# Optimization experiments

Measured on AMD Instinct MI355X. Metric: run time of the kernel, lower is better.

## Reference

```python
import jax, jax.numpy as jnp
import numpy as np

B, S, D = 4, 2048, 1024  # batch, seq_len, input_dim == output_dim (dk)


def setup_inputs() -> dict:
    key = jax.random.key(0)
    kx, kq, kk, kv = jax.random.split(key, 4)
    # xavier_uniform bound for square [D, D] matrices
    bound = float(np.sqrt(6.0 / (D + D)))
    return {
        "x": jax.random.normal(kx, (B, S, D), dtype=jnp.float32),
        "WQ": jax.random.uniform(kq, (D, D), jnp.float32, -bound, bound),
        "WK": jax.random.uniform(kk, (D, D), jnp.float32, -bound, bound),
        "WV": jax.random.uniform(kv, (D, D), jnp.float32, -bound, bound),
    }


def reference(x, WQ, WK, WV):
    dk = WQ.shape[1]
    q = x @ WQ  # [B, S, dk]
    k = x @ WK
    v = x @ WV
    scores = jnp.einsum("bsd,btd->bst", q, k) / jnp.sqrt(jnp.asarray(dk, x.dtype))
    # causal mask: tril ones -> positions where mask==0 set to -inf
    s = x.shape[1]
    causal = jnp.tril(jnp.ones((s, s), dtype=bool))
    scores = jnp.where(causal[None, :, :], scores, jnp.asarray(-jnp.inf, x.dtype))
    attention = jax.nn.softmax(scores, axis=-1)
    # NOTE: original applies attention_dropout to `scores` post-softmax and
    # discards the result -> dead op; eval-mode output is attention @ v.
    return jnp.einsum("bst,btd->bsd", attention, v)
```

## Files before the change

kernel.cpp:

```cpp
#include <hip/hip_runtime.h>
#include <stdint.h>


typedef unsigned short u16;
typedef __attribute__((ext_vector_type(8))) short shortx8;
typedef __attribute__((ext_vector_type(4))) float floatx4;

static constexpr int BB = 4;
static constexpr int SS = 2048;
static constexpr int DD = 1024;

__device__ __forceinline__ u16 f2bf(float f) {
  union { float f; uint32_t u; } c; c.f = f;
  uint32_t u = c.u;
  return (u16)((u + 0x7fffu + ((u >> 16) & 1u)) >> 16);
}

__device__ __forceinline__ float bfhi2f(uint32_t u) {
  union { uint32_t u; float f; } c; c.u = u & 0xffff0000u; return c.f;
}
__device__ __forceinline__ float bflo2f(uint32_t u) {
  union { uint32_t u; float f; } c; c.u = u << 16; return c.f;
}

#define GLOAD_LDS16(g, l)                                                              \
  __builtin_amdgcn_global_load_lds((const __attribute__((address_space(1))) void*)(g), \
                                   (__attribute__((address_space(3))) void*)(l), 16, 0, 0)

__device__ __forceinline__ void gemm_core_128(
    const u16* __restrict__ A, const u16* __restrict__ Bt,
    int lda, int ldb, int m0, int n0, int kend, floatx4 acc[4][4])
{
  __shared__ u16 lA[128 * 64];
  __shared__ u16 lB[128 * 64];
  const int t = threadIdx.x;
  const int w = t >> 6, l = t & 63;
  const int wm = w >> 1, wn = w & 1;
  const int sr = l >> 3;
  const int scq = ((l & 7) ^ (l >> 3)) * 8;

#pragma unroll
  for (int i = 0; i < 4; ++i)
#pragma unroll
    for (int j = 0; j < 4; ++j)
      acc[i][j] = (floatx4){0.f, 0.f, 0.f, 0.f};

  const u16* Ab = A + (size_t)m0 * lda;
  const u16* Bb = Bt + (size_t)n0 * ldb;

  for (int k0 = 0; k0 < kend; k0 += 64) {
#pragma unroll
    for (int i = 0; i < 4; ++i) {
      const int row = w * 32 + i * 8;
      GLOAD_LDS16(Ab + (size_t)(row + sr) * lda + k0 + scq, &lA[row * 64]);
      GLOAD_LDS16(Bb + (size_t)(row + sr) * ldb + k0 + scq, &lB[row * 64]);
    }
    __syncthreads();

#pragma unroll
    for (int ks = 0; ks < 2; ++ks) {
      const int ca = ((ks * 4 + (l >> 4)) ^ (l & 7)) * 8;
      shortx8 af[4], bf[4];
#pragma unroll
      for (int i = 0; i < 4; ++i)
        af[i] = *(const shortx8*)&lA[(wm * 64 + i * 16 + (l & 15)) * 64 + ca];
#pragma unroll
      for (int i = 0; i < 4; ++i)
        bf[i] = *(const shortx8*)&lB[(wn * 64 + i * 16 + (l & 15)) * 64 + ca];
#pragma unroll
      for (int i = 0; i < 4; ++i)
#pragma unroll
        for (int j = 0; j < 4; ++j)
          acc[i][j] = __builtin_amdgcn_mfma_f32_16x16x32_bf16(af[i], bf[j], acc[i][j], 0, 0, 0);
    }
    __syncthreads();
  }
}

__global__ __launch_bounds__(256) void prep(const float* __restrict__ x,
                                            const float* __restrict__ WQ,
                                            const float* __restrict__ WK,
                                            const float* __restrict__ WV,
                                            u16* __restrict__ xb,
                                            u16* __restrict__ Wt) {
  __shared__ float tile[64][65];
  const int bid = blockIdx.x;
  const int t = threadIdx.x;
  if (bid < 8192) {
    const size_t i = (size_t)bid * 256 + t;
    float4 v = ((const float4*)x)[i];
    ushort4 o;
    o.x = f2bf(v.x); o.y = f2bf(v.y); o.z = f2bf(v.z); o.w = f2bf(v.w);
    ((ushort4*)xb)[i] = o;
    return;
  }
  const int r = bid - 8192;
  const int wsel = r >> 8;
  const int rr = r & 255;
  const int k0 = (rr >> 4) * 64, n0 = (rr & 15) * 64;
  const float* W = wsel == 0 ? WQ : (wsel == 1 ? WK : WV);
  const int tx = t & 63, ty = t >> 6;
#pragma unroll
  for (int i = 0; i < 16; ++i)
    tile[ty + i * 4][tx] = W[(size_t)(k0 + ty + i * 4) * DD + n0 + tx];
  __syncthreads();
  u16* dst = Wt + (size_t)wsel * DD * DD;
#pragma unroll
  for (int i = 0; i < 16; ++i)
    dst[(size_t)(n0 + ty + i * 4) * DD + k0 + tx] = f2bf(tile[tx][ty + i * 4]);
}

__global__ __launch_bounds__(256, 2) void qkv_gemm(const u16* __restrict__ x,
                                                   const u16* __restrict__ Wt,
                                                   u16* __restrict__ Q,
                                                   u16* __restrict__ K,
                                                   u16* __restrict__ Vt) {
  const int m0 = blockIdx.x * 128;
  const int n0t = blockIdx.y * 128;
  floatx4 acc[4][4];
  gemm_core_128(x, Wt, DD, DD, m0, n0t, DD, acc);

  const int t = threadIdx.x, w = t >> 6, l = t & 63;
  const int wm = w >> 1, wn = w & 1;

  if (n0t >= 2048) {
    const int bb = m0 >> 11;
    const int s0 = (m0 & 2047) + wm * 64 + (l >> 4) * 4;
    u16* vt = Vt + (size_t)bb * DD * SS;
#pragma unroll
    for (int i = 0; i < 4; ++i)
#pragma unroll
      for (int j = 0; j < 4; ++j) {
        const int n = (n0t - 2048) + wn * 64 + j * 16 + (l & 15);
        const int s = s0 + i * 16;
        ushort4 o4;
        o4.x = f2bf(acc[i][j][0]);
        o4.y = f2bf(acc[i][j][1]);
        o4.z = f2bf(acc[i][j][2]);
        o4.w = f2bf(acc[i][j][3]);
        *(ushort4*)(vt + (size_t)n * SS + s) = o4;
      }
    return;
  }

  u16* out = (n0t < 1024) ? Q : K;
  const int n0 = n0t & 1023;
#pragma unroll
  for (int i = 0; i < 4; ++i)
#pragma unroll
    for (int j = 0; j < 4; ++j)
#pragma unroll
      for (int r = 0; r < 4; ++r) {
        const int m = m0 + wm * 64 + i * 16 + (l >> 4) * 4 + r;
        const int n = n0 + wn * 64 + j * 16 + (l & 15);
        out[(size_t)m * DD + n] = f2bf(acc[i][j][r]);
      }
}

__global__ __launch_bounds__(256, 2) void scores_gemm(const u16* __restrict__ Q,
                                                      const u16* __restrict__ Kt,
                                                      u16* __restrict__ Scb) {
  const int b = blockIdx.z;
  const int tcode = blockIdx.x;
  int mb = (int)((sqrtf(8.0f * (float)tcode + 1.0f) - 1.0f) * 0.5f);
  while ((mb + 1) * (mb + 2) / 2 <= tcode) ++mb;
  while (mb * (mb + 1) / 2 > tcode) --mb;
  const int nb = tcode - mb * (mb + 1) / 2;
  const int m0 = mb * 128, n0 = nb * 128;

  floatx4 acc[4][4];
  gemm_core_128(Q + (size_t)b * SS * DD, Kt + (size_t)b * SS * DD, DD, DD, m0, n0, DD, acc);

  u16* out = Scb + (size_t)b * SS * SS;
  const int t = threadIdx.x, w = t >> 6, l = t & 63;
  const int wm = w >> 1, wn = w & 1;
#pragma unroll
  for (int i = 0; i < 4; ++i)
#pragma unroll
    for (int j = 0; j < 4; ++j)
#pragma unroll
      for (int r = 0; r < 4; ++r) {
        const int m = m0 + wm * 64 + i * 16 + (l >> 4) * 4 + r;
        const int n = n0 + wn * 64 + j * 16 + (l & 15);
        out[(size_t)m * SS + n] = f2bf(acc[i][j][r] * 0.03125f);
      }
}

__global__ __launch_bounds__(256) void softmax_causal(const u16* __restrict__ Scb,
                                                      u16* __restrict__ P) {
  const int row = blockIdx.x * 4 + (threadIdx.x >> 6);
  const int l = threadIdx.x & 63;
  const int b = row >> 11, i = row & 2047;
  const u16* s = Scb + (size_t)b * SS * SS + (size_t)i * SS;
  u16* p = P + (size_t)b * SS * SS + (size_t)i * SS;
  const int n = i + 1;
  const int jend = (i + 128) & ~127;
  const int nc = (jend + 511) >> 9;

  float v[4][8];
  float mx = -INFINITY;
#pragma unroll
  for (int c = 0; c < 4; ++c) {
    if (c < nc) {
      const int col = c * 512 + l * 8;
      uint4 raw = *(const uint4*)(s + col);
      v[c][0] = bflo2f(raw.x); v[c][1] = bfhi2f(raw.x);
      v[c][2] = bflo2f(raw.y); v[c][3] = bfhi2f(raw.y);
      v[c][4] = bflo2f(raw.z); v[c][5] = bfhi2f(raw.z);
      v[c][6] = bflo2f(raw.w); v[c][7] = bfhi2f(raw.w);
#pragma unroll
      for (int e = 0; e < 8; ++e) {
        v[c][e] = (col + e < n) ? v[c][e] : -INFINITY;
        mx = fmaxf(mx, v[c][e]);
      }
    }
  }
#pragma unroll
  for (int o = 32; o > 0; o >>= 1) mx = fmaxf(mx, __shfl_xor(mx, o, 64));

  float sum = 0.f;
#pragma unroll
  for (int c = 0; c < 4; ++c) {
    if (c < nc) {
#pragma unroll
      for (int e = 0; e < 8; ++e) {
        v[c][e] = __expf(v[c][e] - mx);
        sum += v[c][e];
      }
    }
  }
#pragma unroll
  for (int o = 32; o > 0; o >>= 1) sum += __shfl_xor(sum, o, 64);
  const float inv = 1.0f / sum;

#pragma unroll
  for (int c = 0; c < 4; ++c) {
    if (c < nc) {
      const int col = c * 512 + l * 8;
      if (col < jend) {
        uint4 o4;
        o4.x = (uint32_t)f2bf(v[c][0] * inv) | ((uint32_t)f2bf(v[c][1] * inv) << 16);
        o4.y = (uint32_t)f2bf(v[c][2] * inv) | ((uint32_t)f2bf(v[c][3] * inv) << 16);
        o4.z = (uint32_t)f2bf(v[c][4] * inv) | ((uint32_t)f2bf(v[c][5] * inv) << 16);
        o4.w = (uint32_t)f2bf(v[c][6] * inv) | ((uint32_t)f2bf(v[c][7] * inv) << 16);
        *(uint4*)(p + col) = o4;
      }
    }
  }
}

__global__ __launch_bounds__(256, 2) void pv_gemm(const u16* __restrict__ P,
                                                  const u16* __restrict__ Vt,
                                                  float* __restrict__ out) {
  const int b = blockIdx.z;
  const int mb = 15 - blockIdx.y;
  const int m0 = mb * 128, n0 = blockIdx.x * 128;
  floatx4 acc[4][4];
  gemm_core_128(P + (size_t)b * SS * SS, Vt + (size_t)b * DD * SS, SS, SS, m0, n0, m0 + 128, acc);

  float* o = out + (size_t)b * SS * DD;
  const int t = threadIdx.x, w = t >> 6, l = t & 63;
  const int wm = w >> 1, wn = w & 1;
#pragma unroll
  for (int i = 0; i < 4; ++i)
#pragma unroll
    for (int j = 0; j < 4; ++j)
#pragma unroll
      for (int r = 0; r < 4; ++r) {
        const int m = m0 + wm * 64 + i * 16 + (l >> 4) * 4 + r;
        const int n = n0 + wn * 64 + j * 16 + (l & 15);
        o[(size_t)m * DD + n] = acc[i][j][r];
      }
}

extern "C" void kernel_launch(void* const* d_in, const int* in_sizes, int n_in,
                              void* d_out, int out_size, void* d_ws, size_t ws_size,
                              hipStream_t stream) {
  const float* x  = (const float*)d_in[0];
  const float* WQ = (const float*)d_in[1];
  const float* WK = (const float*)d_in[2];
  const float* WV = (const float*)d_in[3];
  float* out = (float*)d_out;

  char* ws = (char*)d_ws;
  const size_t WT_OFF = 0;
  const size_t XB_OFF = WT_OFF + (size_t)3072 * 1024 * 2;
  const size_t Q_OFF  = XB_OFF + (size_t)BB * SS * DD * 2;
  const size_t K_OFF  = Q_OFF + (size_t)BB * SS * DD * 2;
  const size_t VT_OFF = K_OFF + (size_t)BB * SS * DD * 2;
  const size_t P_OFF  = VT_OFF + (size_t)BB * SS * DD * 2;
  const size_t SC_OFF = P_OFF + (size_t)BB * SS * SS * 2;
  u16* Wt  = (u16*)(ws + WT_OFF);
  u16* xb  = (u16*)(ws + XB_OFF);
  u16* Q   = (u16*)(ws + Q_OFF);
  u16* Kb  = (u16*)(ws + K_OFF);
  u16* Vt  = (u16*)(ws + VT_OFF);
  u16* P   = (u16*)(ws + P_OFF);
  u16* Scb = (u16*)(ws + SC_OFF);

  hipLaunchKernelGGL(prep, dim3(8960), dim3(256), 0, stream, x, WQ, WK, WV, xb, Wt);
  hipLaunchKernelGGL(qkv_gemm, dim3(64, 24), dim3(256), 0, stream, xb, Wt, Q, Kb, Vt);
  hipLaunchKernelGGL(scores_gemm, dim3(136, 1, 4), dim3(256), 0, stream, Q, Kb, Scb);
  hipLaunchKernelGGL(softmax_causal, dim3(2048), dim3(256), 0, stream, Scb, P);
  hipLaunchKernelGGL(pv_gemm, dim3(8, 16, 4), dim3(256), 0, stream, P, Vt, out);
}
```

Before: 238.3 us.

## Add 256x256 double-buffered 8-wave GEMM core for QKV and scores kernels

Introduces a 256x256 tile GEMM core with 512 threads, double-buffered LDS staging via global_load_lds, and interleaved quadrant MFMA phases with explicit barriers, waitcnts and setprio. The QKV projection and causal scores kernels switch to it, with grid sizes and the triangular tile indexing adjusted. The goal is more data reuse per tile and overlap of global loads with MFMA work. The cost is 128KB of LDS per block, lower occupancy and coarser causal-tile granularity, which computes more masked work in the scores GEMM.

Result: no change. 239.8 us (+0.6%).

```diff
diff --git a/kernel.cpp b/kernel.cpp
--- a/kernel.cpp
+++ b/kernel.cpp
@@ -23,9 +23,9 @@
   union { uint32_t u; float f; } c; c.u = u << 16; return c.f;
 }
 
-#define GLOAD_LDS16(g, l)                                                              \
-  __builtin_amdgcn_global_load_lds((const __attribute__((address_space(1))) void*)(g), \
-                                   (__attribute__((address_space(3))) void*)(l), 16, 0, 0)
+#define GLOAD_LDS16(g_, l_)                                                             \
+  __builtin_amdgcn_global_load_lds((const __attribute__((address_space(1))) void*)(g_), \
+                                   (__attribute__((address_space(3))) void*)(l_), 16, 0, 0)
 
 __device__ __forceinline__ void gemm_core_128(
     const u16* __restrict__ A, const u16* __restrict__ Bt,
@@ -75,6 +75,132 @@
     }
     __syncthreads();
   }
+}
+
+#define LOAD_AF(mh_)                                                                     \
+  _Pragma("unroll")                                                                      \
+  for (int mi = 0; mi < 4; ++mi)                                                         \
+    _Pragma("unroll")                                                                    \
+    for (int kk = 0; kk < 2; ++kk)                                                       \
+      af[mi][kk] = *(const shortx8*)&As[((mh_) * 128 + wr * 64 + mi * 16 + fr) * 64 +    \
+                                        (((kk * 4 + fq) ^ (l & 7)) * 8)];
+
+#define LOAD_BF(nh_)                                                                     \
+  _Pragma("unroll")                                                                      \
+  for (int ni = 0; ni < 2; ++ni)                                                         \
+    _Pragma("unroll")                                                                    \
+    for (int kk = 0; kk < 2; ++kk)                                                       \
+      bf[ni][kk] = *(const shortx8*)&Bs[((nh_) * 128 + wc * 32 + ni * 16 + fr) * 64 +    \
+                                        (((kk * 4 + fq) ^ (l & 7)) * 8)];
+
+#define MFMA_QUAD(mh_, nh_)                                                              \
+  do {                                                                                   \
+    __builtin_amdgcn_s_setprio(1);                                                       \
+    _Pragma("unroll")                                                                    \
+    for (int mi = 0; mi < 4; ++mi)                                                       \
+      _Pragma("unroll")                                                                  \
+      for (int ni = 0; ni < 2; ++ni)                                                     \
+        _Pragma("unroll")                                                                \
+        for (int kk = 0; kk < 2; ++kk)                                                   \
+          acc[mh_][nh_][mi][ni] = __builtin_amdgcn_mfma_f32_16x16x32_bf16(               \
+              af[mi][kk], bf[ni][kk], acc[mh_][nh_][mi][ni], 0, 0, 0);                   \
+    __builtin_amdgcn_s_setprio(0);                                                       \
+  } while (0)
+
+#define STAGE_A(buf_, half_, k_)                                                         \
+  do {                                                                                   \
+    _Pragma("unroll")                                                                    \
+    for (int j = 0; j < 2; ++j) {                                                        \
+      const int row0 = (half_) * 128 + wv * 16 + j * 8;                                  \
+      GLOAD_LDS16(Ab + (size_t)(row0 + sr) * lda + (k_) + scq, &sm[buf_][0][row0 * 64]); \
+    }                                                                                    \
+  } while (0)
+
+#define STAGE_B(buf_, half_, k_)                                                         \
+  do {                                                                                   \
+    _Pragma("unroll")                                                                    \
+    for (int j = 0; j < 2; ++j) {                                                        \
+      const int row0 = (half_) * 128 + wv * 16 + j * 8;                                  \
+      GLOAD_LDS16(Bb + (size_t)(row0 + sr) * ldb + (k_) + scq, &sm[buf_][1][row0 * 64]); \
+    }                                                                                    \
+  } while (0)
+
+__device__ __forceinline__ void gemm_core_256(
+    const u16* __restrict__ A, const u16* __restrict__ Bt,
+    int lda, int ldb, int m0, int n0, int kend,
+    floatx4 (&acc)[2][2][4][2])
+{
+  __shared__ u16 sm[2][2][256 * 64];
+  const int t = threadIdx.x;
+  const int wv = t >> 6, l = t & 63;
+  const int wr = wv >> 2, wc = wv & 3;
+  const int fr = l & 15, fq = l >> 4;
+  const int sr = l >> 3;
+  const int scq = ((l & 7) ^ sr) * 8;
+
+#pragma unroll
+  for (int a = 0; a < 2; ++a)
+#pragma unroll
+    for (int bq = 0; bq < 2; ++bq)
+#pragma unroll
+      for (int mi = 0; mi < 4; ++mi)
+#pragma unroll
+        for (int ni = 0; ni < 2; ++ni)
+          acc[a][bq][mi][ni] = (floatx4){0.f, 0.f, 0.f, 0.f};
+
+  const u16* Ab = A + (size_t)m0 * lda;
+  const u16* Bb = Bt + (size_t)n0 * ldb;
+  const int T = kend >> 6;
+
+  STAGE_A(0, 0, 0); STAGE_A(0, 1, 0);
+  STAGE_B(0, 0, 0); STAGE_B(0, 1, 0);
+  {
+    const int k1p = (T > 1) ? 64 : 0;
+    STAGE_A(1, 0, k1p);
+    STAGE_B(1, 1, k1p);
+  }
+  asm volatile("s_waitcnt vmcnt(4)" ::: "memory");
+  __builtin_amdgcn_s_barrier();
+
+  shortx8 af[4][2], bf[2][2];
+
+  for (int tt = 0; tt < T; ++tt) {
+    const int c = tt & 1, o = c ^ 1;
+    const u16* As = &sm[c][0][0];
+    const u16* Bs = &sm[c][1][0];
+    const int kn1 = ((tt + 1 < T) ? tt + 1 : T - 1) * 64;
+    const int kn2 = ((tt + 2 < T) ? tt + 2 : T - 1) * 64;
+
+    LOAD_AF(0); LOAD_BF(0);
+    STAGE_A(o, 1, kn1);
+    __builtin_amdgcn_s_barrier();
+    asm volatile("s_waitcnt lgkmcnt(0)" ::: "memory");
+    MFMA_QUAD(0, 0);
+    __builtin_amdgcn_s_barrier();
+
+    LOAD_BF(1);
+    STAGE_B(o, 0, kn1);
+    __builtin_amdgcn_s_barrier();
+    asm volatile("s_waitcnt lgkmcnt(0)" ::: "memory");
+    MFMA_QUAD(0, 1);
+    __builtin_amdgcn_s_barrier();
+
+    LOAD_AF(1);
+    STAGE_A(c, 0, kn2);
+    __builtin_amdgcn_s_barrier();
+    asm volatile("s_waitcnt lgkmcnt(0)" ::: "memory");
+    MFMA_QUAD(1, 1);
+    __builtin_amdgcn_s_barrier();
+
+    LOAD_BF(0);
+    STAGE_B(c, 1, kn2);
+    __builtin_amdgcn_s_barrier();
+    asm volatile("s_waitcnt lgkmcnt(0)" ::: "memory");
+    MFMA_QUAD(1, 0);
+    asm volatile("s_waitcnt vmcnt(4)" ::: "memory");
+    __builtin_amdgcn_s_barrier();
+  }
+  asm volatile("s_waitcnt vmcnt(0)" ::: "memory");
 }
 
 __global__ __launch_bounds__(256) void prep(const float* __restrict__ x,
@@ -110,54 +236,63 @@
     dst[(size_t)(n0 + ty + i * 4) * DD + k0 + tx] = f2bf(tile[tx][ty + i * 4]);
 }
 
-__global__ __launch_bounds__(256, 2) void qkv_gemm(const u16* __restrict__ x,
+__global__ __launch_bounds__(512, 2) void qkv_gemm(const u16* __restrict__ x,
                                                    const u16* __restrict__ Wt,
                                                    u16* __restrict__ Q,
                                                    u16* __restrict__ K,
                                                    u16* __restrict__ Vt) {
-  const int m0 = blockIdx.x * 128;
-  const int n0t = blockIdx.y * 128;
-  floatx4 acc[4][4];
-  gemm_core_128(x, Wt, DD, DD, m0, n0t, DD, acc);
-
-  const int t = threadIdx.x, w = t >> 6, l = t & 63;
-  const int wm = w >> 1, wn = w & 1;
+  const int m0 = blockIdx.x * 256;
+  const int n0t = blockIdx.y * 256;
+  floatx4 acc[2][2][4][2];
+  gemm_core_256(x, Wt, DD, DD, m0, n0t, DD, acc);
+
+  const int t = threadIdx.x, wv = t >> 6, l = t & 63;
+  const int wr = wv >> 2, wc = wv & 3;
+  const int fr = l & 15, fq = l >> 4;
 
   if (n0t >= 2048) {
     const int bb = m0 >> 11;
-    const int s0 = (m0 & 2047) + wm * 64 + (l >> 4) * 4;
     u16* vt = Vt + (size_t)bb * DD * SS;
-#pragma unroll
-    for (int i = 0; i < 4; ++i)
-#pragma unroll
-      for (int j = 0; j < 4; ++j) {
-        const int n = (n0t - 2048) + wn * 64 + j * 16 + (l & 15);
-        const int s = s0 + i * 16;
-        ushort4 o4;
-        o4.x = f2bf(acc[i][j][0]);
-        o4.y = f2bf(acc[i][j][1]);
-        o4.z = f2bf(acc[i][j][2]);
-        o4.w = f2bf(acc[i][j][3]);
-        *(ushort4*)(vt + (size_t)n * SS + s) = o4;
-      }
+    const int sb = m0 & 2047;
+#pragma unroll
+    for (int mh = 0; mh < 2; ++mh)
+#pragma unroll
+      for (int nh = 0; nh < 2; ++nh)
+#pragma unroll
+        for (int mi = 0; mi < 4; ++mi)
+#pragma unroll
+          for (int ni = 0; ni < 2; ++ni) {
+            const int d = (n0t - 2048) + nh * 128 + wc * 32 + ni * 16 + fr;
+            const int s = sb + mh * 128 + wr * 64 + mi * 16 + fq * 4;
+            ushort4 o4;
+            o4.x = f2bf(acc[mh][nh][mi][ni][0]);
+            o4.y = f2bf(acc[mh][nh][mi][ni][1]);
+            o4.z = f2bf(acc[mh][nh][mi][ni][2]);
+            o4.w = f2bf(acc[mh][nh][mi][ni][3]);
+            *(ushort4*)(vt + (size_t)d * SS + s) = o4;
+          }
     return;
   }
 
   u16* out = (n0t < 1024) ? Q : K;
   const int n0 = n0t & 1023;
 #pragma unroll
-  for (int i = 0; i < 4; ++i)
-#pragma unroll
-    for (int j = 0; j < 4; ++j)
-#pragma unroll
-      for (int r = 0; r < 4; ++r) {
-        const int m = m0 + wm * 64 + i * 16 + (l >> 4) * 4 + r;
-        const int n = n0 + wn * 64 + j * 16 + (l & 15);
-        out[(size_t)m * DD + n] = f2bf(acc[i][j][r]);
-      }
-}
-
-__global__ __launch_bounds__(256, 2) void scores_gemm(const u16* __restrict__ Q,
+  for (int mh = 0; mh < 2; ++mh)
+#pragma unroll
+    for (int nh = 0; nh < 2; ++nh)
+#pragma unroll
+      for (int mi = 0; mi < 4; ++mi)
+#pragma unroll
+        for (int ni = 0; ni < 2; ++ni)
+#pragma unroll
+          for (int r = 0; r < 4; ++r) {
+            const int m = m0 + mh * 128 + wr * 64 + mi * 16 + fq * 4 + r;
+            const int n = n0 + nh * 128 + wc * 32 + ni * 16 + fr;
+            out[(size_t)m * DD + n] = f2bf(acc[mh][nh][mi][ni][r]);
+          }
+}
+
+__global__ __launch_bounds__(512, 2) void scores_gemm(const u16* __restrict__ Q,
                                                       const u16* __restrict__ Kt,
                                                       u16* __restrict__ Scb) {
   const int b = blockIdx.z;
@@ -166,24 +301,29 @@
   while ((mb + 1) * (mb + 2) / 2 <= tcode) ++mb;
   while (mb * (mb + 1) / 2 > tcode) --mb;
   const int nb = tcode - mb * (mb + 1) / 2;
-  const int m0 = mb * 128, n0 = nb * 128;
-
-  floatx4 acc[4][4];
-  gemm_core_128(Q + (size_t)b * SS * DD, Kt + (size_t)b * SS * DD, DD, DD, m0, n0, DD, acc);
+  const int m0 = mb * 256, n0 = nb * 256;
+
+  floatx4 acc[2][2][4][2];
+  gemm_core_256(Q + (size_t)b * SS * DD, Kt + (size_t)b * SS * DD, DD, DD, m0, n0, DD, acc);
 
   u16* out = Scb + (size_t)b * SS * SS;
-  const int t = threadIdx.x, w = t >> 6, l = t & 63;
-  const int wm = w >> 1, wn = w & 1;
-#pragma unroll
-  for (int i = 0; i < 4; ++i)
-#pragma unroll
-    for (int j = 0; j < 4; ++j)
-#pragma unroll
-      for (int r = 0; r < 4; ++r) {
-        const int m = m0 + wm * 64 + i * 16 + (l >> 4) * 4 + r;
-        const int n = n0 + wn * 64 + j * 16 + (l & 15);
-        out[(size_t)m * SS + n] = f2bf(acc[i][j][r] * 0.03125f);
-      }
+  const int t = threadIdx.x, wv = t >> 6, l = t & 63;
+  const int wr = wv >> 2, wc = wv & 3;
+  const int fr = l & 15, fq = l >> 4;
+#pragma unroll
+  for (int mh = 0; mh < 2; ++mh)
+#pragma unroll
+    for (int nh = 0; nh < 2; ++nh)
+#pragma unroll
+      for (int mi = 0; mi < 4; ++mi)
+#pragma unroll
+        for (int ni = 0; ni < 2; ++ni)
+#pragma unroll
+          for (int r = 0; r < 4; ++r) {
+            const int m = m0 + mh * 128 + wr * 64 + mi * 16 + fq * 4 + r;
+            const int n = n0 + nh * 128 + wc * 32 + ni * 16 + fr;
+            out[(size_t)m * SS + n] = f2bf(acc[mh][nh][mi][ni][r] * 0.03125f);
+          }
 }
 
 __global__ __launch_bounds__(256) void softmax_causal(const u16* __restrict__ Scb,
@@ -299,8 +439,8 @@
   u16* Scb = (u16*)(ws + SC_OFF);
 
   hipLaunchKernelGGL(prep, dim3(8960), dim3(256), 0, stream, x, WQ, WK, WV, xb, Wt);
-  hipLaunchKernelGGL(qkv_gemm, dim3(64, 24), dim3(256), 0, stream, xb, Wt, Q, Kb, Vt);
-  hipLaunchKernelGGL(scores_gemm, dim3(136, 1, 4), dim3(256), 0, stream, Q, Kb, Scb);
+  hipLaunchKernelGGL(qkv_gemm, dim3(32, 12), dim3(512), 0, stream, xb, Wt, Q, Kb, Vt);
+  hipLaunchKernelGGL(scores_gemm, dim3(36, 1, 4), dim3(512), 0, stream, Q, Kb, Scb);
   hipLaunchKernelGGL(softmax_causal, dim3(2048), dim3(256), 0, stream, Scb, P);
   hipLaunchKernelGGL(pv_gemm, dim3(8, 16, 4), dim3(256), 0, stream, P, Vt, out);
 }
```
